# Kernel tuning notes

Hardware: AMD Instinct MI355X
Metric: run time of the kernel (lower is better)

Reference implementation:

```python
import jax, jax.numpy as jnp
import numpy as np

B, L, D = 2, 2048, 1024
NH, KVH, DH = 16, 8, 64
GROUPS = NH // KVH
ROPE_THETA = 10000.0
SPARSITY = 0.5


def setup_inputs() -> dict:
    key = jax.random.key(0)
    ks = jax.random.split(key, 5)
    hidden_states = jax.random.normal(ks[0], (B, L, D), dtype=jnp.float32)
    wq = jax.random.normal(ks[1], (D, NH * DH), dtype=jnp.float32) * 0.02
    wk = jax.random.normal(ks[2], (D, KVH * DH), dtype=jnp.float32) * 0.02
    wv = jax.random.normal(ks[3], (D, KVH * DH), dtype=jnp.float32) * 0.02
    wo = jax.random.normal(ks[4], (NH * DH, D), dtype=jnp.float32) * 0.02
    position_ids = jnp.broadcast_to(jnp.arange(L, dtype=jnp.int64 if jax.config.jax_enable_x64 else jnp.int32), (B, L))
    return {"hidden_states": hidden_states, "wq": wq, "wk": wk, "wv": wv, "wo": wo,
            "position_ids": position_ids}


def _rope_cos_sin(position_ids, dh, theta):
    inv_freq = 1.0 / (theta ** (jnp.arange(0, dh, 2, dtype=jnp.float32) / dh))  # [dh/2]
    freqs = position_ids.astype(jnp.float32)[..., None] * inv_freq              # [B,L,dh/2]
    emb = jnp.concatenate([freqs, freqs], axis=-1)                              # [B,L,dh]
    return jnp.cos(emb)[:, None], jnp.sin(emb)[:, None]                         # [B,1,L,dh]


def _rotate_half(x):
    h = x.shape[-1] // 2
    return jnp.concatenate([-x[..., h:], x[..., :h]], axis=-1)


def _attention(hidden_states, wq, wk, wv, wo, position_ids):
    b, l, _ = hidden_states.shape
    q = (hidden_states @ wq).reshape(b, l, NH, DH).transpose(0, 2, 1, 3)    # [B,NH,L,DH]
    k = (hidden_states @ wk).reshape(b, l, KVH, DH).transpose(0, 2, 1, 3)   # [B,KVH,L,DH]
    v = (hidden_states @ wv).reshape(b, l, KVH, DH).transpose(0, 2, 1, 3)

    cos, sin = _rope_cos_sin(position_ids, DH, ROPE_THETA)
    q = q * cos + _rotate_half(q) * sin
    k = k * cos + _rotate_half(k) * sin

    # repeat_kv: expand kv heads to match query heads (interleaved like torch)
    k = jnp.repeat(k, GROUPS, axis=1)
    v = jnp.repeat(v, GROUPS, axis=1)

    scale = DH ** -0.5
    scores = jnp.einsum("bhqd,bhkd->bhqk", q, k) * scale                    # [B,NH,L,L]

    # dynamic sparsity: keep exactly top_k entries per row (scatter mask, like torch)
    top_k = max(1, int(SPARSITY * l))
    flat = scores.reshape(-1, l)                                            # [N,L]
    _, idx = jax.lax.top_k(flat, top_k)                                     # [N,k]
    rows = jnp.arange(flat.shape[0])[:, None]
    mask = jnp.zeros(flat.shape, dtype=bool).at[rows, idx].set(True)
    min_val = jnp.finfo(flat.dtype).min
    sparse = jnp.where(mask, flat, min_val).reshape(scores.shape)

    probs = jax.nn.softmax(sparse.astype(jnp.float32), axis=-1).astype(q.dtype)
    out = jnp.einsum("bhqk,bhkd->bhqd", probs, v)                            # [B,NH,L,DH]
    out = out.transpose(0, 2, 1, 3).reshape(b, l, NH * DH)
    return out @ wo


def reference(hidden_states, wq, wk, wv, wo, position_ids):
    return _attention(hidden_states, wq, wk, wv, wo, position_ids)
```

## Files before the change

### kernel.cpp

```cpp
#include <hip/hip_runtime.h>
#include <cstdint>
#include <cstddef>

typedef unsigned int u32;
typedef unsigned long long u64;
typedef __attribute__((ext_vector_type(8))) short s8v;
typedef __attribute__((ext_vector_type(4))) float f4v;
typedef __attribute__((ext_vector_type(4))) unsigned short us4;

#define B_   2
#define L_   2048
#define D_   1024
#define NH_  16
#define KVH_ 8
#define DH_  64
#define TOPK_ 1024

#define MFMA16(a, b, c) __builtin_amdgcn_mfma_f32_16x16x32_bf16(a, b, c, 0, 0, 0)

__device__ __forceinline__ u32 fkey(float s) {
    u32 b = __float_as_uint(s);
    return b ^ ((u32)((int)b >> 31) | 0x80000000u);
}
__device__ __forceinline__ float fkeyinv(u32 k) {
    u32 b = (k & 0x80000000u) ? (k ^ 0x80000000u) : ~k;
    return __uint_as_float(b);
}
__device__ __forceinline__ unsigned short bf16rne(float x) {
    u32 u = __float_as_uint(x);
    u32 r = (u + 0x7FFFu + ((u >> 16) & 1u)) >> 16;
    return (unsigned short)r;
}
__device__ __forceinline__ float bf2f(unsigned short h) {
    return __uint_as_float((u32)h << 16);
}

__global__ __launch_bounds__(256) void prep_wt(const float* __restrict__ W,
                                               unsigned short* __restrict__ WtH,
                                               unsigned short* __restrict__ WtL,
                                               int K, int N) {
    __shared__ float tile[64 * 65];
    int k0 = blockIdx.x * 64, n0 = blockIdx.y * 64;
    int t = threadIdx.x;
#pragma unroll
    for (int i = 0; i < 16; ++i) {
        int idx = t + i * 256;
        int kk = idx >> 6, nn = idx & 63;
        tile[kk * 65 + nn] = W[(size_t)(k0 + kk) * N + n0 + nn];
    }
    __syncthreads();
#pragma unroll
    for (int i = 0; i < 16; ++i) {
        int idx = t + i * 256;
        int nn = idx >> 6, kk = idx & 63;
        float x = tile[kk * 65 + nn];
        unsigned short hi = bf16rne(x);
        unsigned short lo = bf16rne(x - bf2f(hi));
        WtH[(size_t)(n0 + nn) * K + k0 + kk] = hi;
        WtL[(size_t)(n0 + nn) * K + k0 + kk] = lo;
    }
}

__global__ __launch_bounds__(256) void split_a(const float* __restrict__ A,
                                               unsigned short* __restrict__ AH,
                                               unsigned short* __restrict__ AL) {
    size_t tid = (size_t)blockIdx.x * 256 + threadIdx.x;
    float4 v = *(const float4*)(A + tid * 4);
    us4 hv, lv;
    float x[4] = {v.x, v.y, v.z, v.w};
#pragma unroll
    for (int i = 0; i < 4; ++i) {
        unsigned short hi = bf16rne(x[i]);
        hv[i] = hi;
        lv[i] = bf16rne(x[i] - bf2f(hi));
    }
    *(us4*)(AH + tid * 4) = hv;
    *(us4*)(AL + tid * 4) = lv;
}

__global__ __launch_bounds__(256) void gemm_bf(
    const unsigned short* __restrict__ Ah,
    const unsigned short* __restrict__ Al,
    int lda,
    const unsigned short* __restrict__ Wh,
    const unsigned short* __restrict__ Wl,
    float* __restrict__ C, int K, int N) {
    __shared__ __align__(16) unsigned short lAh[128 * 40];
    __shared__ __align__(16) unsigned short lAl[128 * 40];
    __shared__ __align__(16) unsigned short lBh[128 * 40];
    __shared__ __align__(16) unsigned short lBl[128 * 40];
    const int t = threadIdx.x, lane = t & 63, w = t >> 6;
    const int quad = lane >> 4, col = lane & 15;
    const int wm = w >> 1, wn = w & 1;
    const int nwg = gridDim.x * gridDim.y;
    const int lin = blockIdx.y * gridDim.x + blockIdx.x;
    const int swz = (lin & 7) * (nwg >> 3) + (lin >> 3);
    const int bx = swz % gridDim.x, by = swz / gridDim.x;
    const int m0 = bx * 128, n0 = by * 128;
    const int sr = t >> 1, sk = (t & 1) * 16;

    f4v acc[4][4];
#pragma unroll
    for (int i = 0; i < 4; ++i)
#pragma unroll
        for (int j = 0; j < 4; ++j) acc[i][j] = (f4v){0.f, 0.f, 0.f, 0.f};

    for (int k0 = 0; k0 < K; k0 += 32) {
        const unsigned short* ap = Ah + (size_t)(m0 + sr) * lda + k0 + sk;
        const unsigned short* alp = Al + (size_t)(m0 + sr) * lda + k0 + sk;
        s8v a_h0 = *(const s8v*)(ap);
        s8v a_h1 = *(const s8v*)(ap + 8);
        s8v a_l0 = *(const s8v*)(alp);
        s8v a_l1 = *(const s8v*)(alp + 8);
        s8v bh0 = *(const s8v*)(Wh + (size_t)(n0 + sr) * K + k0 + sk);
        s8v bh1 = *(const s8v*)(Wh + (size_t)(n0 + sr) * K + k0 + sk + 8);
        s8v bl0 = *(const s8v*)(Wl + (size_t)(n0 + sr) * K + k0 + sk);
        s8v bl1 = *(const s8v*)(Wl + (size_t)(n0 + sr) * K + k0 + sk + 8);
        __syncthreads();
        *(s8v*)&lAh[sr * 40 + sk]     = a_h0;
        *(s8v*)&lAh[sr * 40 + sk + 8] = a_h1;
        *(s8v*)&lAl[sr * 40 + sk]     = a_l0;
        *(s8v*)&lAl[sr * 40 + sk + 8] = a_l1;
        *(s8v*)&lBh[sr * 40 + sk]     = bh0;
        *(s8v*)&lBh[sr * 40 + sk + 8] = bh1;
        *(s8v*)&lBl[sr * 40 + sk]     = bl0;
        *(s8v*)&lBl[sr * 40 + sk + 8] = bl1;
        __syncthreads();
        s8v amh[4], aml[4], bnh[4], bnl[4];
#pragma unroll
        for (int mt = 0; mt < 4; ++mt) {
            amh[mt] = *(s8v*)&lAh[(wm * 64 + mt * 16 + col) * 40 + quad * 8];
            aml[mt] = *(s8v*)&lAl[(wm * 64 + mt * 16 + col) * 40 + quad * 8];
        }
#pragma unroll
        for (int nt = 0; nt < 4; ++nt) {
            bnh[nt] = *(s8v*)&lBh[(wn * 64 + nt * 16 + col) * 40 + quad * 8];
            bnl[nt] = *(s8v*)&lBl[(wn * 64 + nt * 16 + col) * 40 + quad * 8];
        }
#pragma unroll
        for (int mt = 0; mt < 4; ++mt)
#pragma unroll
            for (int nt = 0; nt < 4; ++nt) {
                acc[mt][nt] = MFMA16(amh[mt], bnh[nt], acc[mt][nt]);
                acc[mt][nt] = MFMA16(amh[mt], bnl[nt], acc[mt][nt]);
                acc[mt][nt] = MFMA16(aml[mt], bnh[nt], acc[mt][nt]);
            }
    }
#pragma unroll
    for (int mt = 0; mt < 4; ++mt)
#pragma unroll
        for (int nt = 0; nt < 4; ++nt)
#pragma unroll
            for (int r = 0; r < 4; ++r)
                C[(size_t)(m0 + wm * 64 + mt * 16 + quad * 4 + r) * N +
                  n0 + wn * 64 + nt * 16 + col] = acc[mt][nt][r];
}

__global__ __launch_bounds__(256) void rope_q(float* __restrict__ Q,
                                              const int* __restrict__ pos) {
    int tid = blockIdx.x * 256 + threadIdx.x;
    int dl = tid & 31;
    int h  = (tid >> 5) & 15;
    int l  = (tid >> 9) & 2047;
    int b  = tid >> 20;
    size_t base = (size_t)(b * L_ + l) * 2048 + h * DH_;
    float x1 = Q[base + dl];
    float x2 = Q[base + dl + 32];
    float p = (float)pos[b * L_ + l];
    float invf = (float)pow(10000.0, -(double)dl / 32.0);
    float a = p * invf;
    float s, c;
    sincosf(a, &s, &c);
    Q[base + dl]      = x1 * c - x2 * s;
    Q[base + dl + 32] = x2 * c + x1 * s;
}

__global__ __launch_bounds__(256) void prep_k(const float* __restrict__ QKV,
                                              unsigned short* __restrict__ KHp,
                                              unsigned short* __restrict__ KLp,
                                              const int* __restrict__ pos) {
    int tid = blockIdx.x * 256 + threadIdx.x;
    int d   = tid & 63;
    int l   = (tid >> 6) & 2047;
    int kvh = (tid >> 17) & 7;
    int b   = tid >> 20;
    size_t src = (size_t)(b * L_ + l) * 2048 + 1024 + kvh * DH_;
    float x  = QKV[src + d];
    int dp   = (d < 32) ? d + 32 : d - 32;
    float xp = QKV[src + dp];
    float p = (float)pos[b * L_ + l];
    int i = d & 31;
    float invf = (float)pow(10000.0, -(double)i / 32.0);
    float a = p * invf;
    float s, c;
    sincosf(a, &s, &c);
    float out = (d < 32) ? (x * c - xp * s) : (x * c + xp * s);
    unsigned short hi = bf16rne(out);
    unsigned short lo = bf16rne(out - bf2f(hi));
    size_t dst = ((size_t)(b * KVH_ + kvh) * L_ + l) * DH_ + d;
    KHp[dst] = hi;
    KLp[dst] = lo;
}

__global__ __launch_bounds__(256) void prep_v(const float* __restrict__ QKV,
                                              unsigned short* __restrict__ VTp) {
    __shared__ float tile[64 * 65];
    int bid = blockIdx.x;
    int lb  = bid & 31;
    int kvh = (bid >> 5) & 7;
    int b   = bid >> 8;
    int l0  = lb * 64;
    int t   = threadIdx.x;
#pragma unroll
    for (int i = 0; i < 16; ++i) {
        int idx = t + i * 256;
        int ll = idx >> 6, d = idx & 63;
        tile[ll * 65 + d] =
            QKV[(size_t)(b * L_ + l0 + ll) * 2048 + 1536 + kvh * DH_ + d];
    }
    __syncthreads();
#pragma unroll
    for (int i = 0; i < 16; ++i) {
        int idx = t + i * 256;
        int d = idx >> 6, ll = idx & 63;
        VTp[((size_t)(b * KVH_ + kvh) * DH_ + d) * L_ + l0 + ll] = bf16rne(tile[ll * 65 + d]);
    }
}

__global__ __launch_bounds__(512, 4) void attn(
    const float* __restrict__ QR,
    const unsigned short* __restrict__ KH,
    const unsigned short* __restrict__ KL,
    const unsigned short* __restrict__ VT,
    unsigned short* __restrict__ AOus) {

    extern __shared__ __align__(16) unsigned char dynsm[];
    float* Sc = (float*)dynsm;
    unsigned short* Pc = (unsigned short*)dynsm;
    u32* hist = (u32*)dynsm;
    float* qtile  = (float*)(dynsm + 66304);
    float* outred = (float*)(dynsm + 66304);

    const int t = threadIdx.x;
    const int lane = t & 63, w = t >> 6;
    const int quad = lane >> 4, col = lane & 15;
    const int bid0 = blockIdx.x;
    const int bid  = (bid0 & 7) * 512 + (bid0 >> 3);
    const int l0  = (bid & 255) * 8;
    const int kvh = (bid >> 8) & 7;
    const int b   = bid >> 11;
    const int r0 = 2 * w, r1 = 2 * w + 1;

    if (t < 256) {
        int q = t >> 4, d4 = (t & 15) * 4;
        *(float4*)&qtile[q * 68 + d4] =
            *(const float4*)(QR + (size_t)(b * L_ + l0 + (q & 7)) * 2048 +
                             (kvh * 2 + (q >> 3)) * DH_ + d4);
    }
    __syncthreads();

    union FR { s8v v; unsigned short u[8]; };
    FR ah[2], al[2];
#pragma unroll
    for (int ks = 0; ks < 2; ++ks)
#pragma unroll
        for (int i = 0; i < 8; ++i) {
            float x = qtile[col * 68 + ks * 32 + quad * 8 + i];
            unsigned short hi = bf16rne(x);
            ah[ks].u[i] = hi;
            al[ks].u[i] = bf16rne(x - bf2f(hi));
        }

    const size_t slabK = (size_t)(b * KVH_ + kvh) * L_ * DH_;
    const unsigned short* khp = KH + slabK;
    const unsigned short* klp = KL + slabK;
    u32 ukA[32], ukB[32];

#pragma unroll
    for (int half = 0; half < 2; ++half) {
        if (half) __syncthreads();
#pragma unroll
        for (int tj = 0; tj < 8; ++tj) {
            int jl = w * 128 + tj * 16;
            int j0 = half * 1024 + jl;
            const unsigned short* kh8 = khp + (size_t)(j0 + col) * 64 + quad * 8;
            const unsigned short* kl8 = klp + (size_t)(j0 + col) * 64 + quad * 8;
            s8v bh0 = *(const s8v*)(kh8);
            s8v bh1 = *(const s8v*)(kh8 + 32);
            s8v bl0 = *(const s8v*)(kl8);
            s8v bl1 = *(const s8v*)(kl8 + 32);
            f4v c = {0.f, 0.f, 0.f, 0.f};
            c = MFMA16(ah[0].v, bh0, c);
            c = MFMA16(al[0].v, bh0, c);
            c = MFMA16(ah[0].v, bl0, c);
            c = MFMA16(ah[1].v, bh1, c);
            c = MFMA16(al[1].v, bh1, c);
            c = MFMA16(ah[1].v, bl1, c);
            c = c * 0.125f;
#pragma unroll
            for (int r = 0; r < 4; ++r)
                Sc[(quad * 4 + r) * 1034 + jl + col] = c[r];
        }
        __syncthreads();
        if (half == 0) {
            outred[t] = 0.f;
            outred[t + 512] = 0.f;
            if (t < 64) outred[1024 + t] = 0.f;
        }
#pragma unroll
        for (int i2 = 0; i2 < 16; ++i2) {
            ukA[half * 16 + i2] = fkey(Sc[r0 * 1034 + i2 * 64 + lane]);
            ukB[half * 16 + i2] = fkey(Sc[r1 * 1034 + i2 * 64 + lane]);
        }
    }
    __syncthreads();

    u32* hq = &hist[w * 1024];
    const int rep = lane & 3;
    auto middle = [&](u32 (&uk)[32]) -> float {
        u32 ulo = 0xFFFFFFFFu, uhi = 0u;
#pragma unroll
        for (int i = 0; i < 32; ++i) {
            u32 u = uk[i];
            ulo = (u < ulo) ? u : ulo;
            uhi = (u > uhi) ? u : uhi;
        }
        for (int off = 1; off < 64; off <<= 1) {
            u32 ol = (u32)__shfl_xor((int)ulo, off);
            u32 oh = (u32)__shfl_xor((int)uhi, off);
            ulo = (ol < ulo) ? ol : ulo;
            uhi = (oh > uhi) ? oh : uhi;
        }
        const float mrow = fkeyinv(uhi);
        const int sh = __clz((int)((uhi - ulo) | 1u));
#pragma unroll
        for (int i = 0; i < 32; ++i) uk[i] = (uk[i] - ulo) << sh;

        u32 pf = 0u, kq = (u32)TOPK_, ng = 0u, geq = 0u;
        for (int pass = 0; pass < 4; ++pass) {
            int shift = 24 - 8 * pass;
#pragma unroll
            for (int i = 0; i < 4; ++i)
                *(uint4*)&hq[i * 256 + lane * 4] = make_uint4(0u, 0u, 0u, 0u);
            u32 pm = pass ? (0xFFFFFFFFu << (shift + 8)) : 0u;
#pragma unroll
            for (int i = 0; i < 32; ++i) {
                u32 u = uk[i];
                if ((u & pm) == pf) {
                    u32 d = (u >> shift) & 255u;
                    atomicAdd(&hq[(d & 3) * 256 + (d >> 2) * 4 + rep], 1u);
                }
            }
            u32 hb_[4];
            u32 s4 = 0u;
#pragma unroll
            for (int bb = 0; bb < 4; ++bb) {
                uint4 hv = *(const uint4*)&hq[bb * 256 + lane * 4];
                hb_[bb] = hv.x + hv.y + hv.z + hv.w;
                s4 += hb_[bb];
            }
            u32 v = s4;
            for (int off = 1; off < 64; off <<= 1) {
                u32 tmp = __shfl_down(v, off);
                if (lane + off < 64) v += tmp;
            }
            u32 g = v - s4;
            u32 mydig = 0u, myk = 0u, myng = 0u, myhb = 0u;
            bool found = false;
#pragma unroll
            for (int bb = 3; bb >= 0; --bb) {
                u32 hb = hb_[bb];
                if (hb && g < kq && kq <= g + hb) {
                    found = true;
                    mydig = (u32)(4 * lane + bb);
                    myk   = kq - g;
                    myng  = ng + g;
                    myhb  = hb;
                }
                g += hb;
            }
            u64 fm = __ballot(found);
            int src = (int)__builtin_ctzll(fm);
            pf |= ((u32)__shfl((int)mydig, src)) << shift;
            kq  = (u32)__shfl((int)myk,  src);
            ng  = (u32)__shfl((int)myng, src);
            u32 hbs = (u32)__shfl((int)myhb, src);
            if (kq == hbs) { geq = 1u; break; }
        }

        const u32 uth = pf;
        u32 selm = 0u;
        if (geq) {
#pragma unroll
            for (int i = 0; i < 32; ++i)
                if (uk[i] >= uth) selm |= 1u << i;
        } else {
            const u32 quota = (u32)TOPK_ - ng;
            u32 eqm = 0u;
#pragma unroll
            for (int i = 0; i < 32; ++i) {
                u32 u = uk[i];
                if (u > uth) selm |= 1u << i;
                else if (u == uth) eqm |= 1u << i;
            }
            u32 ec = (u32)__builtin_popcount(eqm);
            for (int off = 1; off < 64; off <<= 1) ec += __shfl_xor(ec, off);
            if (ec == quota) {
                selm |= eqm;
            } else {
                u32 base = 0;
                u64 lmask = ((u64)1 << lane) - 1;
#pragma unroll
                for (int i = 0; i < 32; ++i) {
                    u64 mm = __ballot((eqm >> i) & 1u);
                    if ((eqm >> i) & 1u) {
                        u32 rk = base + (u32)__builtin_popcountll(mm & lmask);
                        if (rk < quota) selm |= 1u << i;
                    }
                    base += (u32)__builtin_popcountll(mm);
                }
            }
        }

        float z = 0.f;
#pragma unroll
        for (int i = 0; i < 32; ++i) {
            float vv = fkeyinv((uk[i] >> sh) + ulo);
            float e = ((selm >> i) & 1u) ? __expf(vv - mrow) : 0.f;
            uk[i] = __float_as_uint(e);
            z += e;
        }
        for (int off = 1; off < 64; off <<= 1) z += __shfl_xor(z, off);
        return 1.0f / z;
    };

    float invZA = middle(ukA);
    float invZB = middle(ukB);

    const unsigned short* vt = VT + (size_t)(b * KVH_ + kvh) * DH_ * L_;
    const int jb0 = w * 256 + quad * 8;
    s8v pv0 = *(const s8v*)(vt + (size_t)( 0 + col) * L_ + jb0);
    s8v pv1 = *(const s8v*)(vt + (size_t)(16 + col) * L_ + jb0);
    s8v pv2 = *(const s8v*)(vt + (size_t)(32 + col) * L_ + jb0);
    s8v pv3 = *(const s8v*)(vt + (size_t)(48 + col) * L_ + jb0);

    __syncthreads();

#pragma unroll
    for (int i = 0; i < 32; ++i) {
        int jp = 1024 * (i >> 4) + 64 * (i & 15) + lane;
        Pc[r0 * 2072 + jp] = bf16rne(__uint_as_float(ukA[i]) * invZA);
        Pc[r1 * 2072 + jp] = bf16rne(__uint_as_float(ukB[i]) * invZB);
    }
    __syncthreads();

    f4v acc0 = {0.f, 0.f, 0.f, 0.f}, acc1 = acc0, acc2 = acc0, acc3 = acc0;
    {
        s8v ap = *(const s8v*)&Pc[col * 2072 + jb0];
        acc0 = MFMA16(ap, pv0, acc0);
        acc1 = MFMA16(ap, pv1, acc1);
        acc2 = MFMA16(ap, pv2, acc2);
        acc3 = MFMA16(ap, pv3, acc3);
    }
#pragma unroll
    for (int kc = 1; kc < 8; ++kc) {
        int jb = w * 256 + kc * 32 + quad * 8;
        s8v ap = *(const s8v*)&Pc[col * 2072 + jb];
        s8v v0 = *(const s8v*)(vt + (size_t)( 0 + col) * L_ + jb);
        s8v v1 = *(const s8v*)(vt + (size_t)(16 + col) * L_ + jb);
        s8v v2 = *(const s8v*)(vt + (size_t)(32 + col) * L_ + jb);
        s8v v3 = *(const s8v*)(vt + (size_t)(48 + col) * L_ + jb);
        acc0 = MFMA16(ap, v0, acc0);
        acc1 = MFMA16(ap, v1, acc1);
        acc2 = MFMA16(ap, v2, acc2);
        acc3 = MFMA16(ap, v3, acc3);
    }

#pragma unroll
    for (int r = 0; r < 4; ++r) {
        atomicAdd(&outred[(quad * 4 + r) * 68 +  0 + col], acc0[r]);
        atomicAdd(&outred[(quad * 4 + r) * 68 + 16 + col], acc1[r]);
        atomicAdd(&outred[(quad * 4 + r) * 68 + 32 + col], acc2[r]);
        atomicAdd(&outred[(quad * 4 + r) * 68 + 48 + col], acc3[r]);
    }
    __syncthreads();
    if (t < 256) {
        int q = t >> 4, d4 = (t & 15) * 4;
        float4 o = *(float4*)&outred[q * 68 + d4];
        size_t m = (size_t)(b * L_ + l0 + (q & 7));
        int n = (kvh * 2 + (q >> 3)) * DH_ + d4;
        float x[4] = {o.x, o.y, o.z, o.w};
        us4 hv, lv;
#pragma unroll
        for (int i = 0; i < 4; ++i) {
            unsigned short hi = bf16rne(x[i]);
            hv[i] = hi;
            lv[i] = bf16rne(x[i] - bf2f(hi));
        }
        *(us4*)(AOus + m * 4096 + 2048 + n) = hv;
        *(us4*)(AOus + m * 4096 + 3072 + n) = lv;
    }
}

extern "C" void kernel_launch(void* const* d_in, const int* in_sizes, int n_in,
                              void* d_out, int out_size, void* d_ws, size_t ws_size,
                              hipStream_t stream) {
    const float* hs = (const float*)d_in[0];
    const float* wq = (const float*)d_in[1];
    const float* wk = (const float*)d_in[2];
    const float* wv = (const float*)d_in[3];
    const float* wo = (const float*)d_in[4];
    const int*  pos = (const int*)d_in[5];

    float* ws = (float*)d_ws;
    const size_t M1 = 1u << 20;
    float* QKV = ws;
    unsigned short* QKVWh = (unsigned short*)(ws +  8 * M1);
    unsigned short* QKVWl = (unsigned short*)(ws +  9 * M1);
    unsigned short* WoH   = (unsigned short*)(ws + 10 * M1);
    unsigned short* WoL   = (unsigned short*)(ws + 10 * M1 + M1 / 2);
    unsigned short* KH    = (unsigned short*)(ws + 11 * M1);
    unsigned short* KL    = (unsigned short*)(ws + 12 * M1);
    unsigned short* VT    = (unsigned short*)(ws + 13 * M1);
    unsigned short* hsH   = (unsigned short*)(ws + 11 * M1);
    unsigned short* hsL   = (unsigned short*)(ws + 13 * M1);
    float* out = (float*)d_out;

    static bool attr_set = false;
    if (!attr_set) {
        hipFuncSetAttribute((const void*)attn,
                            hipFuncAttributeMaxDynamicSharedMemorySize, 70656);
        attr_set = true;
    }

    dim3 blk(256);
    prep_wt<<<dim3(16, 16), blk, 0, stream>>>(wq, QKVWh, QKVWl, 1024, 1024);
    prep_wt<<<dim3(16,  8), blk, 0, stream>>>(wk, QKVWh + (size_t)1024 * 1024,
                                              QKVWl + (size_t)1024 * 1024, 1024, 512);
    prep_wt<<<dim3(16,  8), blk, 0, stream>>>(wv, QKVWh + (size_t)1536 * 1024,
                                              QKVWl + (size_t)1536 * 1024, 1024, 512);
    prep_wt<<<dim3(16, 16), blk, 0, stream>>>(wo, WoH, WoL, 1024, 1024);
    split_a<<<dim3(4096), blk, 0, stream>>>(hs, hsH, hsL);
    gemm_bf<<<dim3(32, 16), blk, 0, stream>>>(hsH, hsL, 1024, QKVWh, QKVWl,
                                              QKV, 1024, 2048);
    rope_q<<<dim3(8192), blk, 0, stream>>>(QKV, pos);
    prep_k<<<dim3(8192), blk, 0, stream>>>(QKV, KH, KL, pos);
    prep_v<<<dim3(512),  blk, 0, stream>>>(QKV, VT);
    attn<<<dim3(4096), dim3(512), 70656, stream>>>(QKV, KH, KL, VT,
                                                   (unsigned short*)QKV);
    gemm_bf<<<dim3(32, 8), blk, 0, stream>>>((unsigned short*)QKV + 2048,
                                             (unsigned short*)QKV + 3072, 4096,
                                             WoH, WoL, out, 1024, 1024);
}
```

Before: 775.7 us.

## Fuse Q RoPE into attention, merge weight prep, interleave two-row radix select

Merges the four weight transposition/split launches into one kernel and removes the separate Q RoPE pass by applying RoPE to the query tile inside the attention kernel, using a small shared-memory frequency table. The per-row radix top-k selection is restructured to process both rows of a wave together with separate histograms, so atomics and shuffles from the two rows can overlap. This removes launches and a full read/write of Q, at the cost of more registers and slightly more shared memory in the attention kernel.

Measured after the change: 800.7 us. 3.2% more time.

```diff
diff --git a/kernel.cpp b/kernel.cpp
--- a/kernel.cpp
+++ b/kernel.cpp
@@ -35,12 +35,21 @@
     return __uint_as_float((u32)h << 16);
 }
 
-__global__ __launch_bounds__(256) void prep_wt(const float* __restrict__ W,
-                                               unsigned short* __restrict__ WtH,
-                                               unsigned short* __restrict__ WtL,
-                                               int K, int N) {
+__global__ __launch_bounds__(256) void prep_wt_all(
+    const float* __restrict__ wq, const float* __restrict__ wk,
+    const float* __restrict__ wv, const float* __restrict__ wo,
+    unsigned short* __restrict__ QKVWh, unsigned short* __restrict__ QKVWl,
+    unsigned short* __restrict__ WoH, unsigned short* __restrict__ WoL) {
     __shared__ float tile[64 * 65];
-    int k0 = blockIdx.x * 64, n0 = blockIdx.y * 64;
+    const int k0 = blockIdx.x * 64;
+    const int byy = blockIdx.y;
+    const float* W;
+    unsigned short *Dh, *Dl;
+    int N, n0, nrow;
+    if (byy < 16)      { W = wq; N = 1024; n0 = byy * 64;        Dh = QKVWh; Dl = QKVWl; nrow = byy * 64; }
+    else if (byy < 24) { W = wk; N = 512;  n0 = (byy - 16) * 64; Dh = QKVWh; Dl = QKVWl; nrow = 1024 + (byy - 16) * 64; }
+    else if (byy < 32) { W = wv; N = 512;  n0 = (byy - 24) * 64; Dh = QKVWh; Dl = QKVWl; nrow = 1536 + (byy - 24) * 64; }
+    else               { W = wo; N = 1024; n0 = (byy - 32) * 64; Dh = WoH;   Dl = WoL;   nrow = (byy - 32) * 64; }
     int t = threadIdx.x;
 #pragma unroll
     for (int i = 0; i < 16; ++i) {
@@ -56,8 +65,8 @@
         float x = tile[kk * 65 + nn];
         unsigned short hi = bf16rne(x);
         unsigned short lo = bf16rne(x - bf2f(hi));
-        WtH[(size_t)(n0 + nn) * K + k0 + kk] = hi;
-        WtL[(size_t)(n0 + nn) * K + k0 + kk] = lo;
+        Dh[(size_t)(nrow + nn) * 1024 + k0 + kk] = hi;
+        Dl[(size_t)(nrow + nn) * 1024 + k0 + kk] = lo;
     }
 }
 
@@ -154,25 +163,6 @@
             for (int r = 0; r < 4; ++r)
                 C[(size_t)(m0 + wm * 64 + mt * 16 + quad * 4 + r) * N +
                   n0 + wn * 64 + nt * 16 + col] = acc[mt][nt][r];
-}
-
-__global__ __launch_bounds__(256) void rope_q(float* __restrict__ Q,
-                                              const int* __restrict__ pos) {
-    int tid = blockIdx.x * 256 + threadIdx.x;
-    int dl = tid & 31;
-    int h  = (tid >> 5) & 15;
-    int l  = (tid >> 9) & 2047;
-    int b  = tid >> 20;
-    size_t base = (size_t)(b * L_ + l) * 2048 + h * DH_;
-    float x1 = Q[base + dl];
-    float x2 = Q[base + dl + 32];
-    float p = (float)pos[b * L_ + l];
-    float invf = (float)pow(10000.0, -(double)dl / 32.0);
-    float a = p * invf;
-    float s, c;
-    sincosf(a, &s, &c);
-    Q[base + dl]      = x1 * c - x2 * s;
-    Q[base + dl + 32] = x2 * c + x1 * s;
 }
 
 __global__ __launch_bounds__(256) void prep_k(const float* __restrict__ QKV,
@@ -232,6 +222,7 @@
     const unsigned short* __restrict__ KH,
     const unsigned short* __restrict__ KL,
     const unsigned short* __restrict__ VT,
+    const int* __restrict__ pos,
     unsigned short* __restrict__ AOus) {
 
     extern __shared__ __align__(16) unsigned char dynsm[];
@@ -240,6 +231,7 @@
     u32* hist = (u32*)dynsm;
     float* qtile  = (float*)(dynsm + 66304);
     float* outred = (float*)(dynsm + 66304);
+    float* ltab   = (float*)(dynsm + 70656);
 
     const int t = threadIdx.x;
     const int lane = t & 63, w = t >> 6;
@@ -251,11 +243,29 @@
     const int b   = bid >> 11;
     const int r0 = 2 * w, r1 = 2 * w + 1;
 
+    if (t < 32) ltab[t] = (float)pow(10000.0, -(double)t / 32.0);
+
     if (t < 256) {
         int q = t >> 4, d4 = (t & 15) * 4;
         *(float4*)&qtile[q * 68 + d4] =
             *(const float4*)(QR + (size_t)(b * L_ + l0 + (q & 7)) * 2048 +
                              (kvh * 2 + (q >> 3)) * DH_ + d4);
+    }
+    __syncthreads();
+
+    if (t < 128) {
+        int q = t >> 3, dg = (t & 7) * 4;
+        float p = (float)pos[b * L_ + l0 + (q & 7)];
+#pragma unroll
+        for (int dd = 0; dd < 4; ++dd) {
+            int d = dg + dd;
+            float x1 = qtile[q * 68 + d];
+            float x2 = qtile[q * 68 + d + 32];
+            float s, c;
+            sincosf(p * ltab[d], &s, &c);
+            qtile[q * 68 + d]      = x1 * c - x2 * s;
+            qtile[q * 68 + d + 32] = x2 * c + x1 * s;
+        }
     }
     __syncthreads();
 
@@ -315,80 +325,152 @@
     }
     __syncthreads();
 
-    u32* hq = &hist[w * 1024];
+    u32* hqA = &hist[w * 2048];
+    u32* hqB = &hist[w * 2048 + 1024];
     const int rep = lane & 3;
-    auto middle = [&](u32 (&uk)[32]) -> float {
-        u32 ulo = 0xFFFFFFFFu, uhi = 0u;
+    float invZA, invZB;
+    u32 geqA = 0u, geqB = 0u, uthA, uthB, ngA = 0u, ngB = 0u;
+    int shAi, shBi;
+    u32 uloA, uloB;
+    float mrowA, mrowB;
+    {
+        u32 loA = 0xFFFFFFFFu, hiA = 0u, loB = 0xFFFFFFFFu, hiB = 0u;
 #pragma unroll
         for (int i = 0; i < 32; ++i) {
-            u32 u = uk[i];
-            ulo = (u < ulo) ? u : ulo;
-            uhi = (u > uhi) ? u : uhi;
+            u32 a = ukA[i], bb = ukB[i];
+            loA = (a < loA) ? a : loA;  hiA = (a > hiA) ? a : hiA;
+            loB = (bb < loB) ? bb : loB; hiB = (bb > hiB) ? bb : hiB;
         }
         for (int off = 1; off < 64; off <<= 1) {
-            u32 ol = (u32)__shfl_xor((int)ulo, off);
-            u32 oh = (u32)__shfl_xor((int)uhi, off);
-            ulo = (ol < ulo) ? ol : ulo;
-            uhi = (oh > uhi) ? oh : uhi;
-        }
-        const float mrow = fkeyinv(uhi);
-        const int sh = __clz((int)((uhi - ulo) | 1u));
-#pragma unroll
-        for (int i = 0; i < 32; ++i) uk[i] = (uk[i] - ulo) << sh;
-
-        u32 pf = 0u, kq = (u32)TOPK_, ng = 0u, geq = 0u;
+            u32 xa = (u32)__shfl_xor((int)loA, off);
+            u32 ya = (u32)__shfl_xor((int)hiA, off);
+            u32 xb = (u32)__shfl_xor((int)loB, off);
+            u32 yb = (u32)__shfl_xor((int)hiB, off);
+            loA = (xa < loA) ? xa : loA;  hiA = (ya > hiA) ? ya : hiA;
+            loB = (xb < loB) ? xb : loB;  hiB = (yb > hiB) ? yb : hiB;
+        }
+        mrowA = fkeyinv(hiA); mrowB = fkeyinv(hiB);
+        shAi = __clz((int)((hiA - loA) | 1u));
+        shBi = __clz((int)((hiB - loB) | 1u));
+        uloA = loA; uloB = loB;
+#pragma unroll
+        for (int i = 0; i < 32; ++i) {
+            ukA[i] = (ukA[i] - loA) << shAi;
+            ukB[i] = (ukB[i] - loB) << shBi;
+        }
+
+        u32 pfA = 0u, kqA = (u32)TOPK_;
+        u32 pfB = 0u, kqB = (u32)TOPK_;
+        u32 doneA = 0u, doneB = 0u;
         for (int pass = 0; pass < 4; ++pass) {
             int shift = 24 - 8 * pass;
-#pragma unroll
-            for (int i = 0; i < 4; ++i)
-                *(uint4*)&hq[i * 256 + lane * 4] = make_uint4(0u, 0u, 0u, 0u);
+            if (!doneA) {
+#pragma unroll
+                for (int i = 0; i < 4; ++i)
+                    *(uint4*)&hqA[i * 256 + lane * 4] = make_uint4(0u, 0u, 0u, 0u);
+            }
+            if (!doneB) {
+#pragma unroll
+                for (int i = 0; i < 4; ++i)
+                    *(uint4*)&hqB[i * 256 + lane * 4] = make_uint4(0u, 0u, 0u, 0u);
+            }
             u32 pm = pass ? (0xFFFFFFFFu << (shift + 8)) : 0u;
 #pragma unroll
             for (int i = 0; i < 32; ++i) {
-                u32 u = uk[i];
-                if ((u & pm) == pf) {
-                    u32 d = (u >> shift) & 255u;
-                    atomicAdd(&hq[(d & 3) * 256 + (d >> 2) * 4 + rep], 1u);
+                if (!doneA) {
+                    u32 u = ukA[i];
+                    if ((u & pm) == pfA) {
+                        u32 d = (u >> shift) & 255u;
+                        atomicAdd(&hqA[(d & 3) * 256 + (d >> 2) * 4 + rep], 1u);
+                    }
                 }
-            }
-            u32 hb_[4];
-            u32 s4 = 0u;
-#pragma unroll
-            for (int bb = 0; bb < 4; ++bb) {
-                uint4 hv = *(const uint4*)&hq[bb * 256 + lane * 4];
-                hb_[bb] = hv.x + hv.y + hv.z + hv.w;
-                s4 += hb_[bb];
-            }
-            u32 v = s4;
+                if (!doneB) {
+                    u32 u = ukB[i];
+                    if ((u & pm) == pfB) {
+                        u32 d = (u >> shift) & 255u;
+                        atomicAdd(&hqB[(d & 3) * 256 + (d >> 2) * 4 + rep], 1u);
+                    }
+                }
+            }
+            u32 hbA_[4] = {0u, 0u, 0u, 0u}, hbB_[4] = {0u, 0u, 0u, 0u};
+            u32 s4A = 0u, s4B = 0u;
+            if (!doneA) {
+#pragma unroll
+                for (int bb = 0; bb < 4; ++bb) {
+                    uint4 hv = *(const uint4*)&hqA[bb * 256 + lane * 4];
+                    hbA_[bb] = hv.x + hv.y + hv.z + hv.w;
+                    s4A += hbA_[bb];
+                }
+            }
+            if (!doneB) {
+#pragma unroll
+                for (int bb = 0; bb < 4; ++bb) {
+                    uint4 hv = *(const uint4*)&hqB[bb * 256 + lane * 4];
+                    hbB_[bb] = hv.x + hv.y + hv.z + hv.w;
+                    s4B += hbB_[bb];
+                }
+            }
+            u32 vA = s4A, vB = s4B;
             for (int off = 1; off < 64; off <<= 1) {
-                u32 tmp = __shfl_down(v, off);
-                if (lane + off < 64) v += tmp;
-            }
-            u32 g = v - s4;
-            u32 mydig = 0u, myk = 0u, myng = 0u, myhb = 0u;
-            bool found = false;
-#pragma unroll
-            for (int bb = 3; bb >= 0; --bb) {
-                u32 hb = hb_[bb];
-                if (hb && g < kq && kq <= g + hb) {
-                    found = true;
-                    mydig = (u32)(4 * lane + bb);
-                    myk   = kq - g;
-                    myng  = ng + g;
-                    myhb  = hb;
+                u32 ta = __shfl_down(vA, off);
+                u32 tb = __shfl_down(vB, off);
+                if (lane + off < 64) { vA += ta; vB += tb; }
+            }
+            if (!doneA) {
+                u32 g = vA - s4A;
+                u32 mydig = 0u, myk = 0u, myng = 0u, myhb = 0u;
+                bool found = false;
+#pragma unroll
+                for (int bb = 3; bb >= 0; --bb) {
+                    u32 hb = hbA_[bb];
+                    if (hb && g < kqA && kqA <= g + hb) {
+                        found = true;
+                        mydig = (u32)(4 * lane + bb);
+                        myk   = kqA - g;
+                        myng  = ngA + g;
+                        myhb  = hb;
+                    }
+                    g += hb;
                 }
-                g += hb;
-            }
-            u64 fm = __ballot(found);
-            int src = (int)__builtin_ctzll(fm);
-            pf |= ((u32)__shfl((int)mydig, src)) << shift;
-            kq  = (u32)__shfl((int)myk,  src);
-            ng  = (u32)__shfl((int)myng, src);
-            u32 hbs = (u32)__shfl((int)myhb, src);
-            if (kq == hbs) { geq = 1u; break; }
-        }
-
-        const u32 uth = pf;
+                u64 fm = __ballot(found);
+                int src = (int)__builtin_ctzll(fm);
+                pfA |= ((u32)__shfl((int)mydig, src)) << shift;
+                kqA  = (u32)__shfl((int)myk,  src);
+                ngA  = (u32)__shfl((int)myng, src);
+                u32 hbs = (u32)__shfl((int)myhb, src);
+                if (kqA == hbs) { geqA = 1u; doneA = 1u; }
+            }
+            if (!doneB) {
+                u32 g = vB - s4B;
+                u32 mydig = 0u, myk = 0u, myng = 0u, myhb = 0u;
+                bool found = false;
+#pragma unroll
+                for (int bb = 3; bb >= 0; --bb) {
+                    u32 hb = hbB_[bb];
+                    if (hb && g < kqB && kqB <= g + hb) {
+                        found = true;
+                        mydig = (u32)(4 * lane + bb);
+                        myk   = kqB - g;
+                        myng  = ngB + g;
+                        myhb  = hb;
+                    }
+                    g += hb;
+                }
+                u64 fm = __ballot(found);
+                int src = (int)__builtin_ctzll(fm);
+                pfB |= ((u32)__shfl((int)mydig, src)) << shift;
+                kqB  = (u32)__shfl((int)myk,  src);
+                ngB  = (u32)__shfl((int)myng, src);
+                u32 hbs = (u32)__shfl((int)myhb, src);
+                if (kqB == hbs) { geqB = 1u; doneB = 1u; }
+            }
+            if (doneA && doneB) break;
+        }
+        uthA = pfA; uthB = pfB;
+    }
+
+    auto finish = [&](u32 (&uk)[32], u32 uth, u32 geq, u32 ng,
+                      int sh, u32 ulo, float mrow) -> float {
         u32 selm = 0u;
         if (geq) {
 #pragma unroll
@@ -421,7 +503,6 @@
                 }
             }
         }
-
         float z = 0.f;
 #pragma unroll
         for (int i = 0; i < 32; ++i) {
@@ -433,9 +514,8 @@
         for (int off = 1; off < 64; off <<= 1) z += __shfl_xor(z, off);
         return 1.0f / z;
     };
-
-    float invZA = middle(ukA);
-    float invZB = middle(ukB);
+    invZA = finish(ukA, uthA, geqA, ngA, shAi, uloA, mrowA);
+    invZB = finish(ukB, uthB, geqB, ngB, shBi, uloB, mrowB);
 
     const unsigned short* vt = VT + (size_t)(b * KVH_ + kvh) * DH_ * L_;
     const int jb0 = w * 256 + quad * 8;
@@ -529,24 +609,19 @@
     static bool attr_set = false;
     if (!attr_set) {
         hipFuncSetAttribute((const void*)attn,
-                            hipFuncAttributeMaxDynamicSharedMemorySize, 70656);
+                            hipFuncAttributeMaxDynamicSharedMemorySize, 70784);
         attr_set = true;
     }
 
     dim3 blk(256);
-    prep_wt<<<dim3(16, 16), blk, 0, stream>>>(wq, QKVWh, QKVWl, 1024, 1024);
-    prep_wt<<<dim3(16,  8), blk, 0, stream>>>(wk, QKVWh + (size_t)1024 * 1024,
-                                              QKVWl + (size_t)1024 * 1024, 1024, 512);
-    prep_wt<<<dim3(16,  8), blk, 0, stream>>>(wv, QKVWh + (size_t)1536 * 1024,
-                                              QKVWl + (size_t)1536 * 1024, 1024, 512);
-    prep_wt<<<dim3(16, 16), blk, 0, stream>>>(wo, WoH, WoL, 1024, 1024);
+    prep_wt_all<<<dim3(16, 48), blk, 0, stream>>>(wq, wk, wv, wo,
+                                                  QKVWh, QKVWl, WoH, WoL);
     split_a<<<dim3(4096), blk, 0, stream>>>(hs, hsH, hsL);
     gemm_bf<<<dim3(32, 16), blk, 0, stream>>>(hsH, hsL, 1024, QKVWh, QKVWl,
                                               QKV, 1024, 2048);
-    rope_q<<<dim3(8192), blk, 0, stream>>>(QKV, pos);
     prep_k<<<dim3(8192), blk, 0, stream>>>(QKV, KH, KL, pos);
     prep_v<<<dim3(512),  blk, 0, stream>>>(QKV, VT);
-    attn<<<dim3(4096), dim3(512), 70656, stream>>>(QKV, KH, KL, VT,
+    attn<<<dim3(4096), dim3(512), 70784, stream>>>(QKV, KH, KL, VT, pos,
                                                    (unsigned short*)QKV);
     gemm_bf<<<dim3(32, 8), blk, 0, stream>>>((unsigned short*)QKV + 2048,
                                              (unsigned short*)QKV + 3072, 4096,
```
